# Kernel tuning notes

Measured on AMD Instinct MI355X. Metric: run time of the kernel, lower is better.

## Reference

```python
import jax, jax.numpy as jnp
import numpy as np

B, T, D, L, G = 64, 256, 1024, 2, 128


def _sn(W, u):
    # torch.nn.utils.spectral_norm: one power iteration, u/v detached
    u = u / (jnp.linalg.norm(u) + 1e-12)
    v = W.T @ u
    v = v / (jnp.linalg.norm(v) + 1e-12)
    u2 = W @ v
    u2 = u2 / (jnp.linalg.norm(u2) + 1e-12)
    u2 = jax.lax.stop_gradient(u2)
    v = jax.lax.stop_gradient(v)
    return W / (u2 @ (W @ v))


def _cell(x, h, c, Wih, Whh, b):
    gates = x @ Wih.T + h @ Whh.T + b  # [B,4D]; torch gate order i,f,g,o
    i, f, g, o = jnp.split(gates, 4, axis=-1)
    c = jax.nn.sigmoid(f) * c + jax.nn.sigmoid(i) * jnp.tanh(g)
    h = jax.nn.sigmoid(o) * jnp.tanh(c)
    return h, c


def _encoder(x, Wih, Whh, b):
    inp = jnp.swapaxes(x, 0, 1)  # [T,B,D]
    bs = x.shape[0]
    hs, cs = [], []
    for l in range(L):
        W1, W2, bb = Wih[l], Whh[l], b[l]

        def step(carry, xt, W1=W1, W2=W2, bb=bb):
            h, c = _cell(xt, carry[0], carry[1], W1, W2, bb)
            return (h, c), h

        init = (jnp.zeros((bs, D), x.dtype), jnp.zeros((bs, D), x.dtype))
        (hL, cL), inp = jax.lax.scan(step, init, inp)
        hs.append(hL)
        cs.append(cL)
    return jnp.stack(hs), jnp.stack(cs)  # [L,B,D] each


def _vae(h, muW, mub, sgW, sgb, outW, outb, eps):
    mu = jnp.einsum('lbd,lgd->lbg', h, muW) + mub[:, None, :]
    sg = jnp.einsum('lbd,lgd->lbg', h, sgW) + sgb[:, None, :]
    z = mu + eps * jnp.exp(sg)  # reparameterization trick
    out = jnp.einsum('lbg,ldg->lbd', z, outW) + outb[:, None, :]
    return out, mu, sg


def _decoder(init_x, h, c, Wih, Whh, b, length):
    def step(carry, _):
        prev, h, c = carry
        x = prev
        nh, nc = [], []
        for l in range(L):
            hl, cl = _cell(x, h[l], c[l], Wih[l], Whh[l], b[l])
            nh.append(hl)
            nc.append(cl)
            x = hl
        return (x, jnp.stack(nh), jnp.stack(nc)), x

    _, ys = jax.lax.scan(step, (init_x, h, c), None, length=length)
    return jnp.swapaxes(ys, 0, 1)  # [B,T,D]


def setup_inputs() -> dict:
    key = jax.random.key(0)
    ks = iter(jax.random.split(key, 40))
    sD = 1.0 / np.sqrt(D)
    sG = 1.0 / np.sqrt(G)

    def uni(shape, s):
        return jax.random.uniform(next(ks), shape, jnp.float32, -s, s)

    inp = {
        'x': jax.random.normal(next(ks), (B, T, D), jnp.float32),
        'initial': jnp.zeros((1, D), jnp.float32),
        'enc_Wih': uni((L, 4 * D, D), sD), 'enc_Whh': uni((L, 4 * D, D), sD),
        'enc_b': uni((L, 4 * D), sD),
        'enc_u_ih': jax.random.normal(next(ks), (L, 4 * D), jnp.float32),
        'enc_u_hh': jax.random.normal(next(ks), (L, 4 * D), jnp.float32),
        'dec_Wih': uni((L, 4 * D, D), sD), 'dec_Whh': uni((L, 4 * D, D), sD),
        'dec_b': uni((L, 4 * D), sD),
        'dec_u_ih': jax.random.normal(next(ks), (L, 4 * D), jnp.float32),
        'dec_u_hh': jax.random.normal(next(ks), (L, 4 * D), jnp.float32),
        'h_muW': uni((L, G, D), sD), 'h_mub': uni((L, G), sD),
        'h_sgW': uni((L, G, D), sD), 'h_sgb': uni((L, G), sD),
        'h_outW': uni((L, D, G), sG), 'h_outb': uni((L, D), sG),
        'c_muW': uni((L, G, D), sD), 'c_mub': uni((L, G), sD),
        'c_sgW': uni((L, G, D), sD), 'c_sgb': uni((L, G), sD),
        'c_outW': uni((L, D, G), sG), 'c_outb': uni((L, D), sG),
        'eps_h': jax.random.normal(next(ks), (L, B, G), jnp.float32),
        'eps_c': jax.random.normal(next(ks), (L, B, G), jnp.float32),
    }
    return inp


def reference(x, initial, enc_Wih, enc_Whh, enc_b, enc_u_ih, enc_u_hh,
              dec_Wih, dec_Whh, dec_b, dec_u_ih, dec_u_hh,
              h_muW, h_mub, h_sgW, h_sgb, h_outW, h_outb,
              c_muW, c_mub, c_sgW, c_sgb, c_outW, c_outb,
              eps_h, eps_c):
    # spectral-norm reparam of all recurrent weight matrices (per layer)
    eW1 = jax.vmap(_sn)(enc_Wih, enc_u_ih)
    eW2 = jax.vmap(_sn)(enc_Whh, enc_u_hh)
    dW1 = jax.vmap(_sn)(dec_Wih, dec_u_ih)
    dW2 = jax.vmap(_sn)(dec_Whh, dec_u_hh)
    h, c = _encoder(x, eW1, eW2, enc_b)
    h, h_mu, h_sg = _vae(h, h_muW, h_mub, h_sgW, h_sgb, h_outW, h_outb, eps_h)
    c, c_mu, c_sg = _vae(c, c_muW, c_mub, c_sgW, c_sgb, c_outW, c_outb, eps_c)
    init_x = jnp.broadcast_to(initial, (x.shape[0], D))
    out = _decoder(init_x, h, c, dW1, dW2, dec_b, x.shape[1])
    mu = jnp.concatenate([h_mu, c_mu], axis=0)
    sg = jnp.concatenate([h_sg, c_sg], axis=0)
    return out, mu, sg
```

## Files before the change

kernel.cpp:

```cpp
#include <hip/hip_runtime.h>

#define B_  64
#define T_  256
#define D_  1024
#define G_  128
#define FD  4096
#define K2  2048
#define BD  65536
#define NWG 256
#define CL  128

typedef unsigned short u16;
typedef __attribute__((ext_vector_type(8))) short frag8;
typedef __attribute__((ext_vector_type(4))) float f4;
typedef __attribute__((ext_vector_type(4))) int i4;

__device__ __forceinline__ u16 f2b(float f) {
  unsigned u = __float_as_uint(f);
  u += 0x7fffu + ((u >> 16) & 1u);
  return (u16)(u >> 16);
}
__device__ __forceinline__ float b2f(u16 s) {
  return __uint_as_float(((unsigned)s) << 16);
}
__device__ __forceinline__ float sigm(float x) { return 1.0f / (1.0f + __expf(-x)); }

__device__ __forceinline__ void stcoh4(void* p, i4 w) {
  asm volatile("global_store_dwordx4 %0, %1, off sc0 sc1"
               :: "v"(p), "v"(w) : "memory");
}

__device__ __forceinline__ void pollpre(const unsigned* s, int base,
                                        unsigned tgt, unsigned* lf,
                                        unsigned fb, unsigned need,
                                        unsigned& pub) {
  if (pub >= need) return;
  const int l = threadIdx.x & 63;
  for (;;) {
    bool ok = true;
    if (l < 8)
      ok = __hip_atomic_load(&s[(base + l) * CL], __ATOMIC_RELAXED,
                             __HIP_MEMORY_SCOPE_AGENT) >= tgt;
    unsigned long long m = __ballot(ok);
    unsigned p = 0;
    while (p < 4u && ((m >> (2 * p)) & 3ull) == 3ull) ++p;
    if (p > pub) {
      if (l == 0)
        __hip_atomic_store(lf, fb + p, __ATOMIC_RELAXED,
                           __HIP_MEMORY_SCOPE_WORKGROUP);
      pub = p;
    }
    if (pub >= need) break;
    __builtin_amdgcn_s_sleep(1);
  }
  asm volatile("" ::: "memory");
}

__device__ __forceinline__ void poll16_pub(const unsigned* s, unsigned tgt,
                                           unsigned* lf, unsigned val) {
  const int l = threadIdx.x & 63;
  for (;;) {
    bool ok = true;
    if (l < 16)
      ok = __hip_atomic_load(&s[l * CL], __ATOMIC_RELAXED,
                             __HIP_MEMORY_SCOPE_AGENT) >= tgt;
    if (__all(ok)) break;
    __builtin_amdgcn_s_sleep(1);
  }
  if (l == 0)
    __hip_atomic_store(lf, val, __ATOMIC_RELAXED, __HIP_MEMORY_SCOPE_WORKGROUP);
  asm volatile("" ::: "memory");
}

__device__ __forceinline__ void lds_wait(const unsigned* lf, unsigned seq) {
  while (__hip_atomic_load(lf, __ATOMIC_RELAXED,
                           __HIP_MEMORY_SCOPE_WORKGROUP) < seq)
    __builtin_amdgcn_s_sleep(1);
  asm volatile("" ::: "memory");
}

__device__ __forceinline__ void wg_arrive(unsigned* cnt, int line) {
  asm volatile("s_waitcnt vmcnt(0)" ::: "memory");
  __syncthreads();
  if (threadIdx.x == 0)
    __hip_atomic_fetch_add(&cnt[line * CL], 1u, __ATOMIC_RELAXED,
                           __HIP_MEMORY_SCOPE_AGENT);
}

__device__ __forceinline__ void wave_wait16(const unsigned* cnt, unsigned tgt) {
  const int l = threadIdx.x & 63;
  if (l < 16) {
    while (__hip_atomic_load(&cnt[l * CL], __ATOMIC_RELAXED,
                             __HIP_MEMORY_SCOPE_AGENT) < tgt)
      __builtin_amdgcn_s_sleep(2);
  }
  asm volatile("" ::: "memory");
}

__device__ __forceinline__ void fullsync(unsigned* g, unsigned ep, int wg,
                                         bool fenced) {
  if (fenced) __builtin_amdgcn_fence(__ATOMIC_RELEASE, "agent");
  wg_arrive(g, wg & 15);
  wave_wait16(g, ep * 16u);
  __syncthreads();
  if (fenced) {
    __builtin_amdgcn_fence(__ATOMIC_ACQUIRE, "agent");
    __syncthreads();
  }
}

__device__ __forceinline__ void load_weights(const u16* __restrict__ Wg, char* wlds) {
  const int t  = threadIdx.x;
  const int r  = t >> 4;
  const int c0 = t & 15;
  const char* src = (const char*)(Wg + (long)r * K2);
  char* dstrow = wlds + (r << 12);
  const int swz = (r & 7) << 4;
  #pragma unroll
  for (int i = 0; i < 16; ++i) {
    const int cb = (c0 + (i << 4)) << 4;
    frag8 v = *(const frag8*)(src + cb);
    *(frag8*)(dstrow + (cb ^ swz)) = v;
  }
  __syncthreads();
}

__device__ __forceinline__ void cellw(
    const u16* __restrict__ A0, const unsigned* c0p, unsigned t0, int a0half,
    const u16* __restrict__ A1, const unsigned* c1p, unsigned t1,
    const char* wlds, float* gl, unsigned* lsf, unsigned seq,
    float& c_reg, const f4& bias, int ug0,
    u16* __restrict__ hout, float* __restrict__ fout, long fstride)
{
  const int tid = threadIdx.x;
  const int lane = tid & 63, wv = tid >> 6;
  const int mt = wv & 3, ks = wv >> 2;
  const int l15 = lane & 15, lgr = lane >> 4;

  f4 acc0 = (f4){0.f,0.f,0.f,0.f}, acc1 = (f4){0.f,0.f,0.f,0.f};
  const int lbase = (lgr * 64 + mt * 16 + l15) * 8;
  const int kwb = lgr << 4;
  const int swz = (l15 & 7) << 4;
  const char* w0r = wlds + ((long)l15 << 12);
  const char* w1r = wlds + ((long)(16 + l15) << 12);
  const int kk0 = ks * 16;

#define MM1(AP, HB, KK) {                                                      \
    frag8 af = *(const frag8*)((AP) + lbase + (KK) * 2048);                    \
    const int kb = ((HB) + ((KK) << 6) + kwb) ^ swz;                           \
    frag8 b0 = *(const frag8*)(w0r + kb);                                      \
    frag8 b1 = *(const frag8*)(w1r + kb);                                      \
    acc0 = __builtin_amdgcn_mfma_f32_16x16x32_bf16(af, b0, acc0, 0, 0, 0);     \
    acc1 = __builtin_amdgcn_mfma_f32_16x16x32_bf16(af, b1, acc1, 0, 0, 0); }

  if (A1) {
    const int hb1 = (1 - a0half) << 11;
    if (c1p) {
      if (wv == 0) poll16_pub(c1p, t1, &lsf[2], seq);
      else         lds_wait(&lsf[2], seq);
    }
    #pragma unroll 8
    for (int kk = kk0; kk < kk0 + 16; ++kk) MM1(A1, hb1, kk)
  }
  if (A0) {
    const int hb0 = a0half << 11;
    if (c0p) {
      const unsigned fb = 4u * (seq - 1u);
      unsigned* lf = &lsf[ks];
      unsigned pub = 0;
      #pragma unroll
      for (int cl = 0; cl < 4; ++cl) {
        const int cc = ks * 4 + cl;
        if (mt == 0) pollpre(c0p, ks * 8, t0, lf, fb, (unsigned)(cl + 1), pub);
        else         lds_wait(lf, fb + (unsigned)cl + 1u);
        #pragma unroll
        for (int kk = cc * 4; kk < cc * 4 + 4; ++kk) MM1(A0, hb0, kk)
      }
    } else {
      #pragma unroll 8
      for (int kk = kk0; kk < kk0 + 16; ++kk) MM1(A0, hb0, kk)
    }
  }
#undef MM1

  float* g = gl + ks * (64 * 32);
  const int orow = mt * 16 + lgr * 4;
  #pragma unroll
  for (int r = 0; r < 4; ++r) {
    g[(orow + r) * 32 + l15]      = acc0[r];
    g[(orow + r) * 32 + 16 + l15] = acc1[r];
  }
  __syncthreads();

  const int row = tid >> 3, ul = tid & 7;
  f4 p0 = *(const f4*)(gl + row * 32 + ul * 4);
  f4 p1 = *(const f4*)(gl + 64 * 32 + row * 32 + ul * 4);
  float iv = p0.x + p1.x + bias.x;
  float fv = p0.y + p1.y + bias.y;
  float gv = p0.z + p1.z + bias.z;
  float ov = p0.w + p1.w + bias.w;
  float cn = sigm(fv) * c_reg + sigm(iv) * tanhf(gv);
  float hh = sigm(ov) * tanhf(cn);
  c_reg = cn;
  unsigned hv = (unsigned)f2b(hh);
  unsigned a  = hv | (__shfl_xor(hv, 1) << 16);
  unsigned b  = __shfl_xor(a, 2);
  unsigned c2 = __shfl_xor(a, 4);
  unsigned d2 = __shfl_xor(b, 4);
  if (ul == 0) {
    i4 w; w.x = (int)a; w.y = (int)b; w.z = (int)c2; w.w = (int)d2;
    stcoh4(hout + ug0 * 64 + row * 8, w);
  }
  if (fout) fout[(long)row * fstride + ug0 + ul] = hh;
}

__device__ __forceinline__ void vae_wg(
    int bid, char* scr,
    const u16* h0f, const u16* h1f, const float* c0f, const float* c1f,
    const float* hmuW, const float* hmub, const float* hsgW, const float* hsgb,
    const float* houtW, const float* houtb,
    const float* cmuW, const float* cmub, const float* csgW, const float* csgb,
    const float* coutW, const float* coutb,
    const float* eps_h, const float* eps_c,
    float* muo, float* sgo, u16* hd0, u16* hd1, float* cd0, float* cd1)
{
  float* hrow = (float*)scr;
  float* muv  = hrow + 1024;
  float* sgv  = muv + 128;
  float* zz   = sgv + 128;
  const int tid = threadIdx.x;
  const int b = bid & 63, l = (bid >> 6) & 1, s = bid >> 7;

  if (s == 0) {
    const u16* h = l ? h1f : h0f;
    for (int i = tid; i < D_; i += 512)
      hrow[i] = b2f(h[(i >> 3) * 512 + b * 8 + (i & 7)]);
  } else {
    const float* c = (l ? c1f : c0f) + b * D_;
    for (int i = tid; i < D_; i += 512) hrow[i] = c[i];
  }
  __syncthreads();

  const float* muW = (s ? cmuW : hmuW) + (long)l * G_ * D_;
  const float* sgW = (s ? csgW : hsgW) + (long)l * G_ * D_;
  const float* mub = (s ? cmub : hmub) + l * G_;
  const float* sgb = (s ? csgb : hsgb) + l * G_;
  const int wv = tid >> 6, lane = tid & 63;
  for (int oi = wv; oi < 2 * G_; oi += 8) {
    const int g = (oi < G_) ? oi : oi - G_;
    const float* Wr = ((oi < G_) ? muW : sgW) + (long)g * D_;
    float d = 0.f;
    for (int j = lane; j < D_; j += 64) d += Wr[j] * hrow[j];
    for (int off = 1; off < 64; off <<= 1) d += __shfl_xor(d, off);
    if (lane == 0) {
      if (oi < G_) muv[g] = d + mub[g]; else sgv[g] = d + sgb[g];
    }
  }
  __syncthreads();
  if (tid < G_) {
    const int g = tid;
    const float mu = muv[g], sg = sgv[g];
    const float* ep = (s ? eps_c : eps_h) + ((long)l * B_ + b) * G_;
    zz[g] = mu + ep[g] * __expf(sg);
    muo[(long)bid * G_ + g] = mu;
    sgo[(long)bid * G_ + g] = sg;
  }
  __syncthreads();
  const float* oW  = (s ? coutW : houtW) + (long)l * D_ * G_;
  const float* obv = (s ? coutb : houtb) + l * D_;
  for (int i = 0; i < 2; ++i) {
    const int dd = i * 512 + tid;
    float acc = obv[dd];
    const float* Wr = oW + (long)dd * G_;
    #pragma unroll 4
    for (int g = 0; g < G_; ++g) acc += zz[g] * Wr[g];
    if (s == 0) {
      (l ? hd1 : hd0)[(dd >> 3) * 512 + b * 8 + (dd & 7)] = f2b(acc);
    } else {
      (l ? cd1 : cd0)[b * D_ + dd] = acc;
    }
  }
  __syncthreads();
}

__global__ __launch_bounds__(512, 1)
void persist(const u16* __restrict__ Wpe, const u16* __restrict__ Wpd,
             const float* __restrict__ bp,
             const u16* __restrict__ xb, const u16* __restrict__ xd0,
             u16* ring0, u16* ring1,
             float* ce0, float* ce1,
             u16* hd0i, u16* hd1i, float* cd0, float* cd1,
             const float* hmuW, const float* hmub, const float* hsgW, const float* hsgb,
             const float* houtW, const float* houtb,
             const float* cmuW, const float* cmub, const float* csgW, const float* csgb,
             const float* coutW, const float* coutb,
             const float* eps_h, const float* eps_c,
             float* out, float* muo, float* sgo, unsigned* bar)
{
  __shared__ __align__(16) char smem[147456 + 64];
  char*  wlds = smem;
  float* gl   = (float*)(smem + 131072);
  unsigned* lsf = (unsigned*)(smem + 147456);

  unsigned* gcnt = bar;
  unsigned* acnt = bar + 2048;
  unsigned* bcnt = bar + 4096;
  unsigned* ccnt = bar + 6144;
  unsigned* dcnt = bar + 8192;

  const int wg  = blockIdx.x;
  const bool isL0 = (wg < 128);
  const int wgL = wg & 127;
  const int ug0 = wgL * 8;
  const int tid = threadIdx.x;
  const int aline = wgL >> 3;

  if (tid == 0) { lsf[0] = 0; lsf[1] = 0; lsf[2] = 0; }
  load_weights(Wpe + (isL0 ? 0l : (long)FD * K2) + (long)wgL * 32 * K2, wlds);
  f4 bias = *(const f4*)(bp + (isL0 ? 0 : FD) + (ug0 + (tid & 7)) * 4);
  float c_reg = 0.f;

  if (isL0) {
    for (int s = 0; s < T_; ++s) {
      cellw(s ? (ring0 + (long)(s - 1) * BD) : nullptr,
            s ? acnt : nullptr, 8u * (unsigned)s, 1,
            xb + (long)s * BD, nullptr, 0,
            wlds, gl, lsf, (unsigned)(s + 1),
            c_reg, bias, ug0,
            ring0 + (long)s * BD, nullptr, 0);
      wg_arrive(acnt, aline);
    }
  } else {
    for (int t = 0; t < T_; ++t) {
      cellw(ring0 + (long)t * BD, acnt, 8u * (unsigned)(t + 1), 0,
            t ? (ring1 + (long)(t - 1) * BD) : nullptr,
            t ? bcnt : nullptr, 8u * (unsigned)t,
            wlds, gl, lsf, (unsigned)(t + 1),
            c_reg, bias, ug0,
            ring1 + (long)t * BD, nullptr, 0);
      wg_arrive(bcnt, aline);
    }
  }
  {
    const int row = tid >> 3, ul = tid & 7;
    (isL0 ? ce0 : ce1)[row * D_ + ug0 + ul] = c_reg;
  }
  fullsync(gcnt, 1, wg, true);

  vae_wg(wg, (char*)gl,
         ring0 + 255l * BD, ring1 + 255l * BD, ce0, ce1,
         hmuW, hmub, hsgW, hsgb, houtW, houtb,
         cmuW, cmub, csgW, csgb, coutW, coutb,
         eps_h, eps_c, muo, sgo, hd0i, hd1i, cd0, cd1);
  fullsync(gcnt, 2, wg, true);

  if (tid == 0) { lsf[0] = 0; lsf[1] = 0; lsf[2] = 0; }
  load_weights(Wpd + (isL0 ? 0l : (long)FD * K2) + (long)wgL * 32 * K2, wlds);
  bias = *(const f4*)(bp + 2 * FD + (isL0 ? 0 : FD) + (ug0 + (tid & 7)) * 4);
  {
    const int row = tid >> 3, ul = tid & 7;
    c_reg = (isL0 ? cd0 : cd1)[row * D_ + ug0 + ul];
  }

  if (isL0) {
    for (int t = 0; t < T_; ++t) {
      cellw(t ? (ring1 + (long)(t - 1) * BD) : xd0,
            t ? dcnt : nullptr, 8u * (unsigned)t, 0,
            t ? (ring0 + (long)(t - 1) * BD) : hd0i,
            t ? ccnt : nullptr, 8u * (unsigned)t,
            wlds, gl, lsf, (unsigned)(t + 1),
            c_reg, bias, ug0,
            ring0 + (long)t * BD, nullptr, 0);
      wg_arrive(ccnt, aline);
    }
  } else {
    for (int t = 0; t < T_; ++t) {
      cellw(ring0 + (long)t * BD, ccnt, 8u * (unsigned)(t + 1), 0,
            t ? (ring1 + (long)(t - 1) * BD) : hd1i,
            t ? dcnt : nullptr, 8u * (unsigned)t,
            wlds, gl, lsf, (unsigned)(t + 1),
            c_reg, bias, ug0,
            ring1 + (long)t * BD, out + (long)t * D_, (long)T_ * D_);
      wg_arrive(dcnt, aline);
    }
  }
}

__device__ __forceinline__ const float* selW(int m, const float* a, const float* b,
                                             const float* c, const float* d) {
  const float* W;
  switch (m >> 1) { case 0: W = a; break; case 1: W = b; break;
                    case 2: W = c; break; default: W = d; }
  return W + (long)(m & 1) * FD * D_;
}
__device__ __forceinline__ const float* selU(int m, const float* a, const float* b,
                                             const float* c, const float* d) {
  const float* u;
  switch (m >> 1) { case 0: u = a; break; case 1: u = b; break;
                    case 2: u = c; break; default: u = d; }
  return u + (m & 1) * FD;
}

__global__ __launch_bounds__(256)
void k_unorm(const float* euih, const float* euhh, const float* duih, const float* duhh,
             float* uinv)
{
  const int m = blockIdx.x;
  const float* u = selU(m, euih, euhh, duih, duhh);
  float s = 0.f;
  for (int i = threadIdx.x; i < FD; i += 256) { float v = u[i]; s += v * v; }
  __shared__ float red[4];
  for (int off = 1; off < 64; off <<= 1) s += __shfl_xor(s, off);
  if ((threadIdx.x & 63) == 0) red[threadIdx.x >> 6] = s;
  __syncthreads();
  if (threadIdx.x == 0)
    uinv[m] = 1.0f / (sqrtf(red[0] + red[1] + red[2] + red[3]) + 1e-12f);
}

__global__ __launch_bounds__(256)
void k_v(const float* eWih, const float* eWhh, const float* dWih, const float* dWhh,
         const float* euih, const float* euhh, const float* duih, const float* duhh,
         const float* uinv, float* v, float* vss)
{
  __shared__ float us[FD];
  __shared__ float red[4];
  const int m = blockIdx.x >> 2, cb = blockIdx.x & 3;
  const float* W = selW(m, eWih, eWhh, dWih, dWhh);
  const float* u = selU(m, euih, euhh, duih, duhh);
  for (int i = threadIdx.x; i < FD; i += 256) us[i] = u[i];
  __syncthreads();
  const int j = cb * 256 + threadIdx.x;
  float acc = 0.f;
  for (int i = 0; i < FD; ++i) acc += W[(long)i * D_ + j] * us[i];
  acc *= uinv[m];
  v[m * D_ + j] = acc;
  float s = acc * acc;
  for (int off = 1; off < 64; off <<= 1) s += __shfl_xor(s, off);
  if ((threadIdx.x & 63) == 0) red[threadIdx.x >> 6] = s;
  __syncthreads();
  if (threadIdx.x == 0) vss[blockIdx.x] = red[0] + red[1] + red[2] + red[3];
}

__global__ __launch_bounds__(256)
void k_sig(const float* eWih, const float* eWhh, const float* dWih, const float* dWhh,
           const float* v, float* sgp)
{
  __shared__ float vl[D_];
  __shared__ float red[4];
  const int m = blockIdx.x >> 6, rb = blockIdx.x & 63;
  const float* W = selW(m, eWih, eWhh, dWih, dWhh);
  for (int i = threadIdx.x; i < D_; i += 256) vl[i] = v[m * D_ + i];
  __syncthreads();
  const int wv = threadIdx.x >> 6, lane = threadIdx.x & 63;
  float ssq = 0.f;
  for (int rr = 0; rr < 16; ++rr) {
    const int r = rb * 64 + wv * 16 + rr;
    const float* Wr = W + (long)r * D_;
    float d = 0.f;
    for (int j = lane; j < D_; j += 64) d += Wr[j] * vl[j];
    for (int off = 1; off < 64; off <<= 1) d += __shfl_xor(d, off);
    ssq += d * d;
  }
  if (lane == 0) red[wv] = ssq;
  __syncthreads();
  if (threadIdx.x == 0) sgp[blockIdx.x] = red[0] + red[1] + red[2] + red[3];
}

__global__ void k_fin(const float* vss, const float* sgp, float* rsig)
{
  const int m = threadIdx.x;
  if (m < 8) {
    float vn = sqrtf(vss[m * 4] + vss[m * 4 + 1] + vss[m * 4 + 2] + vss[m * 4 + 3]);
    float s2 = 0.f;
    for (int i = 0; i < 64; ++i) s2 += sgp[m * 64 + i];
    rsig[m] = (vn + 1e-12f) / sqrtf(s2);
  }
}

__global__ __launch_bounds__(256)
void k_pack(const float* eWih, const float* eWhh, const float* dWih, const float* dWhh,
            const float* rsig, u16* Wpe, u16* Wpd)
{
  const long idx = (long)blockIdx.x * 256 + threadIdx.x;
  const int k8   = (int)(idx & 255);
  const int np   = (int)((idx >> 8) & 4095);
  const int pair = (int)(idx >> 20);
  const int l = pair & 1, ed = pair >> 1;
  const int u = np >> 2, g = np & 3;
  const int srow = g * D_ + u;
  const int k = k8 * 8;
  const float* src; float sc;
  if (k < D_) {
    const float* Wih = ed ? dWih : eWih;
    src = Wih + ((long)(l * FD + srow)) * D_ + k;
    sc  = rsig[ed ? 4 + l : l];
  } else {
    const float* Whh = ed ? dWhh : eWhh;
    src = Whh + ((long)(l * FD + srow)) * D_ + (k - D_);
    sc  = rsig[ed ? 6 + l : 2 + l];
  }
  f4 a = *(const f4*)src;
  f4 b = *(const f4*)(src + 4);
  frag8 o;
  o[0] = (short)f2b(a.x * sc); o[1] = (short)f2b(a.y * sc);
  o[2] = (short)f2b(a.z * sc); o[3] = (short)f2b(a.w * sc);
  o[4] = (short)f2b(b.x * sc); o[5] = (short)f2b(b.y * sc);
  o[6] = (short)f2b(b.z * sc); o[7] = (short)f2b(b.w * sc);
  u16* dst = (ed ? Wpd : Wpe) + ((long)(l * FD + np)) * K2 + k;
  *(frag8*)dst = o;
}

__global__ void k_packb(const float* eb, const float* db, float* bp)
{
  const int idx = blockIdx.x * 256 + threadIdx.x;
  const int j = idx & 4095, pair = idx >> 12;
  const int l = pair & 1, ed = pair >> 1;
  const float* b = (ed ? db : eb) + l * FD;
  bp[pair * FD + j] = b[(j & 3) * D_ + (j >> 2)];
}

__global__ __launch_bounds__(512)
void k_xb(const float* __restrict__ x, u16* __restrict__ xb)
{
  const long i8 = ((long)blockIdx.x * 512 + threadIdx.x) * 8;
  const int t   = (int)(i8 >> 16);
  const int rem = (int)(i8 & 65535);
  const int m   = rem >> 9;
  const int b   = (rem >> 3) & 63;
  const float* src = x + ((long)b * T_ + t) * D_ + m * 8;
  f4 a = *(const f4*)src;
  f4 c = *(const f4*)(src + 4);
  frag8 o;
  o[0] = (short)f2b(a.x); o[1] = (short)f2b(a.y);
  o[2] = (short)f2b(a.z); o[3] = (short)f2b(a.w);
  o[4] = (short)f2b(c.x); o[5] = (short)f2b(c.y);
  o[6] = (short)f2b(c.z); o[7] = (short)f2b(c.w);
  *(frag8*)(xb + i8) = o;
}

__global__ __launch_bounds__(512)
void k_xd0(const float* __restrict__ initial, u16* __restrict__ xd0)
{
  const int i8 = (blockIdx.x * 512 + threadIdx.x) * 8;
  const int m  = i8 >> 9;
  f4 a = *(const f4*)(initial + m * 8);
  f4 c = *(const f4*)(initial + m * 8 + 4);
  frag8 o;
  o[0] = (short)f2b(a.x); o[1] = (short)f2b(a.y);
  o[2] = (short)f2b(a.z); o[3] = (short)f2b(a.w);
  o[4] = (short)f2b(c.x); o[5] = (short)f2b(c.y);
  o[6] = (short)f2b(c.z); o[7] = (short)f2b(c.w);
  *(frag8*)(xd0 + i8) = o;
}

extern "C" void kernel_launch(void* const* d_in, const int* in_sizes, int n_in,
                              void* d_out, int out_size, void* d_ws, size_t ws_size,
                              hipStream_t stream)
{
  const float* x       = (const float*)d_in[0];
  const float* initial = (const float*)d_in[1];
  const float* eWih    = (const float*)d_in[2];
  const float* eWhh    = (const float*)d_in[3];
  const float* eb      = (const float*)d_in[4];
  const float* euih    = (const float*)d_in[5];
  const float* euhh    = (const float*)d_in[6];
  const float* dWih    = (const float*)d_in[7];
  const float* dWhh    = (const float*)d_in[8];
  const float* db      = (const float*)d_in[9];
  const float* duih    = (const float*)d_in[10];
  const float* duhh    = (const float*)d_in[11];
  const float* hmuW    = (const float*)d_in[12];
  const float* hmub    = (const float*)d_in[13];
  const float* hsgW    = (const float*)d_in[14];
  const float* hsgb    = (const float*)d_in[15];
  const float* houtW   = (const float*)d_in[16];
  const float* houtb   = (const float*)d_in[17];
  const float* cmuW    = (const float*)d_in[18];
  const float* cmub    = (const float*)d_in[19];
  const float* csgW    = (const float*)d_in[20];
  const float* csgb    = (const float*)d_in[21];
  const float* coutW   = (const float*)d_in[22];
  const float* coutb   = (const float*)d_in[23];
  const float* eps_h   = (const float*)d_in[24];
  const float* eps_c   = (const float*)d_in[25];

  char* w = (char*)d_ws;
  auto alloc = [&](size_t n) -> char* {
    char* p = w; w += (n + 255) & ~(size_t)255; return p;
  };
  u16*   Wpe   = (u16*)  alloc(2l * FD * K2 * 2);
  u16*   Wpd   = (u16*)  alloc(2l * FD * K2 * 2);
  u16*   xb    = (u16*)  alloc((long)T_ * BD * 2);
  u16*   ring0 = (u16*)  alloc((long)T_ * BD * 2);
  u16*   ring1 = (u16*)  alloc((long)T_ * BD * 2);
  u16*   xd0   = (u16*)  alloc((long)BD * 2);
  u16*   hd0i  = (u16*)  alloc((long)BD * 2);
  u16*   hd1i  = (u16*)  alloc((long)BD * 2);
  float* ce0   = (float*)alloc((long)BD * 4);
  float* ce1   = (float*)alloc((long)BD * 4);
  float* cd0   = (float*)alloc((long)BD * 4);
  float* cd1   = (float*)alloc((long)BD * 4);
  float* bp    = (float*)alloc(4l * FD * 4);
  float* vv    = (float*)alloc(8l * D_ * 4);
  float* uinv  = (float*)alloc(64);
  float* vss   = (float*)alloc(256);
  float* sgp   = (float*)alloc(4096);
  float* rsig  = (float*)alloc(64);
  unsigned* bar = (unsigned*)alloc(40960);

  hipMemsetAsync(bar, 0, 40960, stream);

  k_unorm<<<8,    256, 0, stream>>>(euih, euhh, duih, duhh, uinv);
  k_v    <<<32,   256, 0, stream>>>(eWih, eWhh, dWih, dWhh, euih, euhh, duih, duhh,
                                    uinv, vv, vss);
  k_sig  <<<512,  256, 0, stream>>>(eWih, eWhh, dWih, dWhh, vv, sgp);
  k_fin  <<<1,    64,  0, stream>>>(vss, sgp, rsig);
  k_pack <<<16384,256, 0, stream>>>(eWih, eWhh, dWih, dWhh, rsig, Wpe, Wpd);
  k_packb<<<64,   256, 0, stream>>>(eb, db, bp);
  k_xb   <<<4096, 512, 0, stream>>>(x, xb);
  k_xd0  <<<16,   512, 0, stream>>>(initial, xd0);

  float* out = (float*)d_out;
  float* muo = out + (long)B_ * T_ * D_;
  float* sgo = muo + 4l * B_ * G_;

  persist<<<NWG, 512, 0, stream>>>(Wpe, Wpd, bp, xb, xd0,
                                   ring0, ring1,
                                   ce0, ce1, hd0i, hd1i, cd0, cd1,
                                   hmuW, hmub, hsgW, hsgb, houtW, houtb,
                                   cmuW, cmub, csgW, csgb, coutW, coutb,
                                   eps_h, eps_c, out, muo, sgo, bar);
}
```

Measured before the change: 4.770 ms.

## Chunk own-layer h polling and drop redundant decoder recurrent waits

Replaces the all-16-counter wait before the recurrent-h matmul with per-chunk polling, so MFMA work on early chunks can start before every workgroup has arrived. In the decoder, the explicit wait on the layer's own previous h is removed. That dependency is instead covered transitively by pre-polling the first chunk of the other layer's counter, whose completion implies the own-layer step is done. This cuts global-atomic polling and serialization on the critical recurrent path. The cost is a correctness argument that rests on the ordering between layers, plus an extra LDS flag slot.

Result: slower. 6.528 ms (+36.8%).

```diff
diff --git a/kernel.cpp b/kernel.cpp
--- a/kernel.cpp
+++ b/kernel.cpp
@@ -56,22 +56,6 @@
   asm volatile("" ::: "memory");
 }
 
-__device__ __forceinline__ void poll16_pub(const unsigned* s, unsigned tgt,
-                                           unsigned* lf, unsigned val) {
-  const int l = threadIdx.x & 63;
-  for (;;) {
-    bool ok = true;
-    if (l < 16)
-      ok = __hip_atomic_load(&s[l * CL], __ATOMIC_RELAXED,
-                             __HIP_MEMORY_SCOPE_AGENT) >= tgt;
-    if (__all(ok)) break;
-    __builtin_amdgcn_s_sleep(1);
-  }
-  if (l == 0)
-    __hip_atomic_store(lf, val, __ATOMIC_RELAXED, __HIP_MEMORY_SCOPE_WORKGROUP);
-  asm volatile("" ::: "memory");
-}
-
 __device__ __forceinline__ void lds_wait(const unsigned* lf, unsigned seq) {
   while (__hip_atomic_load(lf, __ATOMIC_RELAXED,
                            __HIP_MEMORY_SCOPE_WORKGROUP) < seq)
@@ -127,7 +111,7 @@
 
 __device__ __forceinline__ void cellw(
     const u16* __restrict__ A0, const unsigned* c0p, unsigned t0, int a0half,
-    const u16* __restrict__ A1, const unsigned* c1p, unsigned t1,
+    const u16* __restrict__ A1, const unsigned* c1p, unsigned t1, int pre01,
     const char* wlds, float* gl, unsigned* lsf, unsigned seq,
     float& c_reg, const f4& bias, int ug0,
     u16* __restrict__ hout, float* __restrict__ fout, long fstride)
@@ -144,6 +128,10 @@
   const char* w0r = wlds + ((long)l15 << 12);
   const char* w1r = wlds + ((long)(16 + l15) << 12);
   const int kk0 = ks * 16;
+  const unsigned fb = 4u * (seq - 1u);
+  unsigned* lf0 = &lsf[ks];
+  unsigned* lf1 = &lsf[2 + ks];
+  unsigned pub0 = 0;
 
 #define MM1(AP, HB, KK) {                                                      \
     frag8 af = *(const frag8*)((AP) + lbase + (KK) * 2048);                    \
@@ -153,26 +141,35 @@
     acc0 = __builtin_amdgcn_mfma_f32_16x16x32_bf16(af, b0, acc0, 0, 0, 0);     \
     acc1 = __builtin_amdgcn_mfma_f32_16x16x32_bf16(af, b1, acc1, 0, 0, 0); }
 
+  if (pre01 && A0 && c0p) {
+    if (mt == 0) pollpre(c0p, ks * 8, t0, lf0, fb, 1u, pub0);
+    else         lds_wait(lf0, fb + 1u);
+  }
   if (A1) {
     const int hb1 = (1 - a0half) << 11;
     if (c1p) {
-      if (wv == 0) poll16_pub(c1p, t1, &lsf[2], seq);
-      else         lds_wait(&lsf[2], seq);
-    }
-    #pragma unroll 8
-    for (int kk = kk0; kk < kk0 + 16; ++kk) MM1(A1, hb1, kk)
+      unsigned pub1 = 0;
+      #pragma unroll
+      for (int cl = 0; cl < 4; ++cl) {
+        if (mt == 0) pollpre(c1p, ks * 8, t1, lf1, fb, (unsigned)(cl + 1), pub1);
+        else         lds_wait(lf1, fb + (unsigned)cl + 1u);
+        const int cc = ks * 4 + cl;
+        #pragma unroll
+        for (int kk = cc * 4; kk < cc * 4 + 4; ++kk) MM1(A1, hb1, kk)
+      }
+    } else {
+      #pragma unroll 8
+      for (int kk = kk0; kk < kk0 + 16; ++kk) MM1(A1, hb1, kk)
+    }
   }
   if (A0) {
     const int hb0 = a0half << 11;
     if (c0p) {
-      const unsigned fb = 4u * (seq - 1u);
-      unsigned* lf = &lsf[ks];
-      unsigned pub = 0;
       #pragma unroll
       for (int cl = 0; cl < 4; ++cl) {
+        if (mt == 0) pollpre(c0p, ks * 8, t0, lf0, fb, (unsigned)(cl + 1), pub0);
+        else         lds_wait(lf0, fb + (unsigned)cl + 1u);
         const int cc = ks * 4 + cl;
-        if (mt == 0) pollpre(c0p, ks * 8, t0, lf, fb, (unsigned)(cl + 1), pub);
-        else         lds_wait(lf, fb + (unsigned)cl + 1u);
         #pragma unroll
         for (int kk = cc * 4; kk < cc * 4 + 4; ++kk) MM1(A0, hb0, kk)
       }
@@ -315,7 +312,7 @@
   const int tid = threadIdx.x;
   const int aline = wgL >> 3;
 
-  if (tid == 0) { lsf[0] = 0; lsf[1] = 0; lsf[2] = 0; }
+  if (tid == 0) { lsf[0]=0; lsf[1]=0; lsf[2]=0; lsf[3]=0; }
   load_weights(Wpe + (isL0 ? 0l : (long)FD * K2) + (long)wgL * 32 * K2, wlds);
   f4 bias = *(const f4*)(bp + (isL0 ? 0 : FD) + (ug0 + (tid & 7)) * 4);
   float c_reg = 0.f;
@@ -324,7 +321,7 @@
     for (int s = 0; s < T_; ++s) {
       cellw(s ? (ring0 + (long)(s - 1) * BD) : nullptr,
             s ? acnt : nullptr, 8u * (unsigned)s, 1,
-            xb + (long)s * BD, nullptr, 0,
+            xb + (long)s * BD, nullptr, 0, 0,
             wlds, gl, lsf, (unsigned)(s + 1),
             c_reg, bias, ug0,
             ring0 + (long)s * BD, nullptr, 0);
@@ -334,7 +331,7 @@
     for (int t = 0; t < T_; ++t) {
       cellw(ring0 + (long)t * BD, acnt, 8u * (unsigned)(t + 1), 0,
             t ? (ring1 + (long)(t - 1) * BD) : nullptr,
-            t ? bcnt : nullptr, 8u * (unsigned)t,
+            t ? bcnt : nullptr, 8u * (unsigned)t, 0,
             wlds, gl, lsf, (unsigned)(t + 1),
             c_reg, bias, ug0,
             ring1 + (long)t * BD, nullptr, 0);
@@ -354,7 +351,7 @@
          eps_h, eps_c, muo, sgo, hd0i, hd1i, cd0, cd1);
   fullsync(gcnt, 2, wg, true);
 
-  if (tid == 0) { lsf[0] = 0; lsf[1] = 0; lsf[2] = 0; }
+  if (tid == 0) { lsf[0]=0; lsf[1]=0; lsf[2]=0; lsf[3]=0; }
   load_weights(Wpd + (isL0 ? 0l : (long)FD * K2) + (long)wgL * 32 * K2, wlds);
   bias = *(const f4*)(bp + 2 * FD + (isL0 ? 0 : FD) + (ug0 + (tid & 7)) * 4);
   {
@@ -367,7 +364,7 @@
       cellw(t ? (ring1 + (long)(t - 1) * BD) : xd0,
             t ? dcnt : nullptr, 8u * (unsigned)t, 0,
             t ? (ring0 + (long)(t - 1) * BD) : hd0i,
-            t ? ccnt : nullptr, 8u * (unsigned)t,
+            nullptr, 0, 1,
             wlds, gl, lsf, (unsigned)(t + 1),
             c_reg, bias, ug0,
             ring0 + (long)t * BD, nullptr, 0);
@@ -377,7 +374,7 @@
     for (int t = 0; t < T_; ++t) {
       cellw(ring0 + (long)t * BD, ccnt, 8u * (unsigned)(t + 1), 0,
             t ? (ring1 + (long)(t - 1) * BD) : hd1i,
-            t ? dcnt : nullptr, 8u * (unsigned)t,
+            nullptr, 0, 1,
             wlds, gl, lsf, (unsigned)(t + 1),
             c_reg, bias, ug0,
             ring1 + (long)t * BD, out + (long)t * D_, (long)T_ * D_);
```
